# Optimization experiments

Measured on AMD Instinct MI355X. Metric: run time of the kernel, lower is better.

The kernel has to match this reference:

```python
import jax, jax.numpy as jnp
import numpy as np

B, T, HW = 16, 64, 7
D = 768          # input_dim == base_dim
N = 12           # num_heads
C = D // N       # head_dim = 64
EPS = 1e-5


def layernorm(x, g, b):
    m = jnp.mean(x, axis=-1, keepdims=True)
    v = jnp.mean((x - m) ** 2, axis=-1, keepdims=True)
    return (x - m) * jax.lax.rsqrt(v + EPS) * g + b


def setup_inputs() -> dict:
    key = jax.random.key(0)
    ks = jax.random.split(key, 12)
    s = lambda k, shape: (jax.random.normal(k, shape, jnp.float32) * 0.02)
    return {
        "x": jax.random.normal(ks[0], (B, T, HW, HW, D), jnp.float32),
        "W_qkv": s(ks[1], (D, 3 * D)),                  # qkv_bias=False
        "Wpq": s(ks[2], (C, C, HW, HW)), "bpq": jnp.zeros((C,), jnp.float32),
        "Wpk": s(ks[3], (C, C, HW, HW)), "bpk": jnp.zeros((C,), jnp.float32),
        "Wpv": s(ks[4], (C, C, HW, HW)), "bpv": jnp.zeros((C,), jnp.float32),
        "g_q": jnp.ones((C,), jnp.float32), "be_q": jnp.zeros((C,), jnp.float32),
        "g_k": jnp.ones((C,), jnp.float32), "be_k": jnp.zeros((C,), jnp.float32),
        "g_v": jnp.ones((C,), jnp.float32), "be_v": jnp.zeros((C,), jnp.float32),
        "rel_pos_t": s(ks[5], (2 * T - 1, C)),          # (127, 64): matches dt, no interp
        "W_proj": s(ks[6], (D, D)), "b_proj": jnp.zeros((D,), jnp.float32),
    }


def reference(x, W_qkv, Wpq, bpq, Wpk, bpk, Wpv, bpv,
              g_q, be_q, g_k, be_k, g_v, be_v, rel_pos_t, W_proj, b_proj):
    b, t = x.shape[0], x.shape[1]
    # qkv projection -> (B,T,H,W,3,N,C)
    qkv = (x @ W_qkv).reshape(b, t, HW, HW, 3, N, C)
    q3, k3, v3 = qkv[..., 0, :, :], qkv[..., 1, :, :], qkv[..., 2, :, :]  # (B,T,H,W,N,C)
    # Conv3d kernel (1,7,7) on full 7x7 spatial == contraction over (h,w,c_in)
    q = jnp.einsum('bthwnc,dchw->bntd', q3, Wpq) + bpq   # (B,N,T,C)
    k = jnp.einsum('bthwnc,dchw->bntd', k3, Wpk) + bpk
    v = jnp.einsum('bthwnc,dchw->bntd', v3, Wpv) + bpv
    q = layernorm(q, g_q, be_q)
    k = layernorm(k, g_k, be_k)
    v = layernorm(v, g_v, be_v)
    scale = C ** -0.5
    attn = jnp.einsum('bntc,bnsc->bnts', q * scale, k)   # (B,N,T,T)
    # relative temporal position bias: gather table rows by distance, matmul with q
    dist = jnp.arange(t)[:, None] - jnp.arange(t)[None, :] + (t - 1)  # (T,T) in [0,2T-2]
    Rt = rel_pos_t[dist]                                  # (T,T,C)
    rel = jnp.einsum('bntc,tsc->bnts', q, Rt)
    attn = jax.nn.softmax(attn + rel, axis=-1)
    out = jnp.einsum('bnts,bnsc->bntc', attn, v) + q      # residual add of q
    out = out.transpose(0, 2, 1, 3).reshape(b, t, N * C)  # (B,T,D)
    return out @ W_proj + b_proj
```

## Files before the change

kernel.cpp:

```cpp
#include <hip/hip_runtime.h>


typedef __attribute__((ext_vector_type(8))) short bf16x8;
typedef __attribute__((ext_vector_type(4))) float f32x4;

#define AS1U(p) ((const __attribute__((address_space(1))) unsigned int*)(p))
#define AS3U(p) ((__attribute__((address_space(3))) unsigned int*)(p))

__device__ __forceinline__ unsigned short cvt_bf16(float x) {
  union { float f; unsigned int u; } v; v.f = x;
  unsigned int r = v.u + 0x7fffu + ((v.u >> 16) & 1u);
  return (unsigned short)(r >> 16);
}
__device__ __forceinline__ float bf2f(unsigned short h) {
  union { unsigned int u; float f; } v; v.u = ((unsigned int)h) << 16;
  return v.f;
}

__global__ __launch_bounds__(256) void cvt_x_k(const float* __restrict__ src,
                                               unsigned short* __restrict__ dst, int n8) {
  int i = blockIdx.x * 256 + threadIdx.x;
  if (i >= n8) return;
  const float4* s = (const float4*)src + (size_t)i * 2;
  float4 a = s[0], b = s[1];
  ushort4 r0 = { cvt_bf16(a.x), cvt_bf16(a.y), cvt_bf16(a.z), cvt_bf16(a.w) };
  ushort4 r1 = { cvt_bf16(b.x), cvt_bf16(b.y), cvt_bf16(b.z), cvt_bf16(b.w) };
  ushort4* d = (ushort4*)dst + (size_t)i * 2;
  d[0] = r0; d[1] = r1;
}

__global__ __launch_bounds__(256) void transpose_cvt_k(const float* __restrict__ src,
                                                       unsigned short* __restrict__ dst) {
  __shared__ float tl[32][33];
  int k0 = blockIdx.x * 32, n0 = blockIdx.y * 32;
  int tx = threadIdx.x & 31, ty = threadIdx.x >> 5;
#pragma unroll
  for (int r = 0; r < 32; r += 8)
    tl[ty + r][tx] = src[(size_t)(k0 + ty + r) * 2304 + n0 + tx];
  __syncthreads();
#pragma unroll
  for (int r = 0; r < 32; r += 8)
    dst[(size_t)(n0 + ty + r) * 768 + k0 + tx] = cvt_bf16(tl[tx][ty + r]);
}

__global__ __launch_bounds__(256) void wp_cvt_k(const float* __restrict__ src,
                                                unsigned short* __restrict__ dst) {
  int o = blockIdx.x * 256 + threadIdx.x;
  if (o >= 204800) return;
  int c = o & 63, d = (o >> 6) & 63, hw = o >> 12;
  dst[o] = (hw < 49) ? cvt_bf16(src[d * 3136 + c * 49 + hw]) : (unsigned short)0;
}

__global__ __launch_bounds__(256) void relp_cvt_k(const float* __restrict__ src,
                                                  unsigned short* __restrict__ dst) {
  int i = blockIdx.x * 256 + threadIdx.x;
  if (i >= 8192) return;
  dst[i] = (i < 8128) ? cvt_bf16(src[i]) : (unsigned short)0;
}

__global__ __launch_bounds__(256) void gemm_qkv_k(
    const unsigned short* __restrict__ A, const unsigned short* __restrict__ Bt,
    unsigned short* __restrict__ Cb) {
  __shared__ unsigned short As[128 * 32];
  __shared__ unsigned short Bs[128 * 32];
  const int L = blockIdx.x;
  const int xcd = L & 7;
  const int slot = L >> 3;
  const int nb = slot % 18;
  const int mb = xcd * 49 + slot / 18;
  const int m0 = mb * 128, n0 = nb * 128;
  const int K = 768, Nn = 2304;

  const int tid = threadIdx.x;
  const int wave = tid >> 6, lane = tid & 63;
  const int quad = lane >> 4, l16 = lane & 15;
  const int wm = (wave >> 1) * 64, wn = (wave & 1) * 64;

  const int srow = lane >> 2;
  const int scol = (lane & 3) * 8;
  const unsigned short* Ag0 = A + (size_t)(m0 + wave * 16 + srow) * K + scol;
  const unsigned short* Ag1 = Ag0 + (size_t)64 * K;
  const unsigned short* Bg0 = Bt + (size_t)(n0 + wave * 16 + srow) * K + scol;
  const unsigned short* Bg1 = Bg0 + (size_t)64 * K;
  unsigned short* Asw0 = &As[(wave * 16) * 32];
  unsigned short* Asw1 = &As[(64 + wave * 16) * 32];
  unsigned short* Bsw0 = &Bs[(wave * 16) * 32];
  unsigned short* Bsw1 = &Bs[(64 + wave * 16) * 32];

  f32x4 acc[4][4];
#pragma unroll
  for (int i = 0; i < 4; ++i)
#pragma unroll
    for (int j = 0; j < 4; ++j) acc[i][j] = (f32x4){0.f, 0.f, 0.f, 0.f};

  for (int k0 = 0; k0 < K; k0 += 32) {
    __builtin_amdgcn_global_load_lds(AS1U(Ag0 + k0), AS3U(Asw0), 16, 0, 0);
    __builtin_amdgcn_global_load_lds(AS1U(Ag1 + k0), AS3U(Asw1), 16, 0, 0);
    __builtin_amdgcn_global_load_lds(AS1U(Bg0 + k0), AS3U(Bsw0), 16, 0, 0);
    __builtin_amdgcn_global_load_lds(AS1U(Bg1 + k0), AS3U(Bsw1), 16, 0, 0);
    __syncthreads();
    bf16x8 af[4], bfr[4];
#pragma unroll
    for (int f = 0; f < 4; ++f) {
      af[f]  = *(const bf16x8*)&As[(wm + f * 16 + l16) * 32 + quad * 8];
      bfr[f] = *(const bf16x8*)&Bs[(wn + f * 16 + l16) * 32 + quad * 8];
    }
#pragma unroll
    for (int i = 0; i < 4; ++i)
#pragma unroll
      for (int j = 0; j < 4; ++j)
        acc[i][j] = __builtin_amdgcn_mfma_f32_16x16x32_bf16(af[i], bfr[j], acc[i][j], 0, 0, 0);
    __syncthreads();
  }

#pragma unroll
  for (int i = 0; i < 4; ++i)
#pragma unroll
    for (int j = 0; j < 4; ++j)
#pragma unroll
      for (int r = 0; r < 4; ++r) {
        int row = m0 + wm + i * 16 + quad * 4 + r;
        int col = n0 + wn + j * 16 + l16;
        Cb[(size_t)row * Nn + col] = cvt_bf16(acc[i][j][r]);
      }
}

__global__ __launch_bounds__(256) void pool_ln_mfma_k(
    const unsigned short* __restrict__ qkvb, const unsigned short* __restrict__ WpTT,
    const float* __restrict__ bq, const float* __restrict__ bk, const float* __restrict__ bv,
    const float* __restrict__ gq, const float* __restrict__ gk, const float* __restrict__ gv,
    const float* __restrict__ beq, const float* __restrict__ bek, const float* __restrict__ bev,
    unsigned short* __restrict__ oq, unsigned short* __restrict__ ok_,
    unsigned short* __restrict__ ov) {
  __shared__ unsigned short As[64 * 128];
  __shared__ unsigned short Bs[64 * 128];
  __shared__ float Ln[64 * 65];
  __shared__ float mu_s[64], rs_s[64];

  const int n = blockIdx.x, p = blockIdx.y, b = blockIdx.z;
  const int tid = threadIdx.x;
  const int wave = tid >> 6, lane = tid & 63;
  const int quad = lane >> 4, l16 = lane & 15;
  const int wm = (wave >> 1) * 32, wn = (wave & 1) * 32;

  const int lr = lane >> 4, lg = lane & 15;
  const size_t abase = ((size_t)b * 3136) * 2304 + (size_t)p * 768 + (size_t)n * 64;
  const unsigned short* WpB = WpTT + (size_t)p * 204800;

  const unsigned short* pA[4];
  const unsigned short* pB[4];
#pragma unroll
  for (int q = 0; q < 4; ++q) {
    int r = wave * 16 + q * 4 + lr;
    int g = lg ^ (r & 15);
    pA[q] = qkvb + abase + (size_t)r * 112896 + (size_t)(g >> 3) * 2304 + (g & 7) * 8;
    pB[q] = WpB + (size_t)(g >> 3) * 4096 + r * 64 + (g & 7) * 8;
  }

  f32x4 acc[2][2];
#pragma unroll
  for (int i = 0; i < 2; ++i)
#pragma unroll
    for (int j = 0; j < 2; ++j) acc[i][j] = (f32x4){0.f, 0.f, 0.f, 0.f};

  for (int it = 0; it < 25; ++it) {
    const size_t offA = (size_t)it * 4608;
    const size_t offB = (size_t)it * 8192;
#pragma unroll
    for (int q = 0; q < 4; ++q) {
      __builtin_amdgcn_global_load_lds(AS1U(pA[q] + offA), AS3U(&As[(wave * 16 + q * 4) * 128]), 16, 0, 0);
      __builtin_amdgcn_global_load_lds(AS1U(pB[q] + offB), AS3U(&Bs[(wave * 16 + q * 4) * 128]), 16, 0, 0);
    }
    __syncthreads();
    bf16x8 af[2][4], bfr[2][4];
#pragma unroll
    for (int f = 0; f < 2; ++f) {
      int ra = wm + f * 16 + l16;
      int rb = wn + f * 16 + l16;
#pragma unroll
      for (int ki = 0; ki < 4; ++ki) {
        af[f][ki]  = *(const bf16x8*)&As[ra * 128 + (((ki * 4 + quad) ^ (ra & 15)) * 8)];
        bfr[f][ki] = *(const bf16x8*)&Bs[rb * 128 + (((ki * 4 + quad) ^ (rb & 15)) * 8)];
      }
    }
#pragma unroll
    for (int ki = 0; ki < 4; ++ki)
#pragma unroll
      for (int i = 0; i < 2; ++i)
#pragma unroll
        for (int j = 0; j < 2; ++j)
          acc[i][j] = __builtin_amdgcn_mfma_f32_16x16x32_bf16(af[i][ki], bfr[j][ki], acc[i][j], 0, 0, 0);
    __syncthreads();
  }

  const float* bias = (p == 0) ? bq : (p == 1) ? bk : bv;
  const float* g    = (p == 0) ? gq : (p == 1) ? gk : gv;
  const float* be   = (p == 0) ? beq : (p == 1) ? bek : bev;
  unsigned short* outp = (p == 0) ? oq : (p == 1) ? ok_ : ov;

#pragma unroll
  for (int i = 0; i < 2; ++i)
#pragma unroll
    for (int j = 0; j < 2; ++j)
#pragma unroll
      for (int r = 0; r < 4; ++r) {
        int t = wm + i * 16 + quad * 4 + r;
        int d = wn + j * 16 + l16;
        Ln[t * 65 + d] = acc[i][j][r] + bias[d];
      }
  __syncthreads();
  if (tid < 64) {
    float s = 0.f;
#pragma unroll 8
    for (int c = 0; c < 64; ++c) s += Ln[tid * 65 + c];
    float m = s * (1.f / 64.f);
    float v2 = 0.f;
#pragma unroll 8
    for (int c = 0; c < 64; ++c) { float dl = Ln[tid * 65 + c] - m; v2 += dl * dl; }
    mu_s[tid] = m;
    rs_s[tid] = rsqrtf(v2 * (1.f / 64.f) + 1e-5f);
  }
  __syncthreads();
  {
    int t = tid >> 2, d0 = (tid & 3) * 16;
    float m = mu_s[t], rv = rs_s[t];
    unsigned short ob[16];
#pragma unroll
    for (int j = 0; j < 16; ++j)
      ob[j] = cvt_bf16((Ln[t * 65 + d0 + j] - m) * rv * g[d0 + j] + be[d0 + j]);
    unsigned short* dst = outp + ((size_t)(b * 12 + n) * 64 + t) * 64 + d0;
    *(uint4*)dst = *(uint4*)ob;
    *(uint4*)(dst + 8) = *(uint4*)(ob + 8);
  }
}

__global__ __launch_bounds__(256) void attn_mfma_k(
    const unsigned short* __restrict__ qp, const unsigned short* __restrict__ kp,
    const unsigned short* __restrict__ vp, const unsigned short* __restrict__ relb,
    float* __restrict__ aout) {
  __shared__ unsigned short qs[64 * 64];
  __shared__ unsigned short ks[64 * 64];
  __shared__ unsigned short vt[64 * 64];
  __shared__ unsigned short rs[128 * 64];
  __shared__ float Gs[64 * 128];
  __shared__ unsigned short Ps[64 * 64];

  const int n = blockIdx.x, b = blockIdx.y;
  const int tid = threadIdx.x;
  const size_t base = ((size_t)b * 12 + n) * 4096;

  for (int i = tid; i < 512; i += 256) {
    ((uint4*)qs)[i] = ((const uint4*)(qp + base))[i];
    ((uint4*)ks)[i] = ((const uint4*)(kp + base))[i];
  }
  for (int i = tid; i < 1024; i += 256)
    ((uint4*)rs)[i] = ((const uint4*)relb)[i];
  {
    int s = tid >> 2, c0 = (tid & 3) * 16;
    unsigned short tmp[16];
    *(uint4*)tmp = *(const uint4*)(vp + base + s * 64 + c0);
    *(uint4*)(tmp + 8) = *(const uint4*)(vp + base + s * 64 + c0 + 8);
#pragma unroll
    for (int i = 0; i < 16; ++i) vt[(c0 + i) * 64 + s] = tmp[i];
  }
  __syncthreads();

  const int wave = tid >> 6, lane = tid & 63;
  const int quad = lane >> 4, l16 = lane & 15;
  const int tm = wave * 16;

  bf16x8 aq[2];
  aq[0] = *(const bf16x8*)&qs[(tm + l16) * 64 + quad * 8];
  aq[1] = *(const bf16x8*)&qs[(tm + l16) * 64 + quad * 8 + 32];

  f32x4 accqk[4], accg[8];
#pragma unroll
  for (int j = 0; j < 4; ++j) accqk[j] = (f32x4){0.f, 0.f, 0.f, 0.f};
#pragma unroll
  for (int j = 0; j < 8; ++j) accg[j] = (f32x4){0.f, 0.f, 0.f, 0.f};

#pragma unroll
  for (int ki = 0; ki < 2; ++ki) {
#pragma unroll
    for (int j = 0; j < 4; ++j) {
      bf16x8 bk = *(const bf16x8*)&ks[(j * 16 + l16) * 64 + quad * 8 + ki * 32];
      accqk[j] = __builtin_amdgcn_mfma_f32_16x16x32_bf16(aq[ki], bk, accqk[j], 0, 0, 0);
    }
#pragma unroll
    for (int j = 0; j < 8; ++j) {
      bf16x8 br = *(const bf16x8*)&rs[(j * 16 + l16) * 64 + quad * 8 + ki * 32];
      accg[j] = __builtin_amdgcn_mfma_f32_16x16x32_bf16(aq[ki], br, accg[j], 0, 0, 0);
    }
  }
#pragma unroll
  for (int j = 0; j < 8; ++j)
#pragma unroll
    for (int r = 0; r < 4; ++r)
      Gs[(tm + quad * 4 + r) * 128 + j * 16 + l16] = accg[j][r];
  __syncthreads();

#pragma unroll
  for (int r = 0; r < 4; ++r) {
    int t = tm + quad * 4 + r;
    float sv[4];
#pragma unroll
    for (int j = 0; j < 4; ++j) {
      int s = j * 16 + l16;
      sv[j] = 0.125f * accqk[j][r] + Gs[t * 128 + (t + 63 - s)];
    }
    float m = fmaxf(fmaxf(sv[0], sv[1]), fmaxf(sv[2], sv[3]));
    m = fmaxf(m, __shfl_xor(m, 1));
    m = fmaxf(m, __shfl_xor(m, 2));
    m = fmaxf(m, __shfl_xor(m, 4));
    m = fmaxf(m, __shfl_xor(m, 8));
    float e[4], sum = 0.f;
#pragma unroll
    for (int j = 0; j < 4; ++j) { e[j] = __expf(sv[j] - m); sum += e[j]; }
    sum += __shfl_xor(sum, 1);
    sum += __shfl_xor(sum, 2);
    sum += __shfl_xor(sum, 4);
    sum += __shfl_xor(sum, 8);
    float inv = 1.f / sum;
#pragma unroll
    for (int j = 0; j < 4; ++j)
      Ps[t * 64 + j * 16 + l16] = cvt_bf16(e[j] * inv);
  }
  __syncthreads();

  bf16x8 ap[2];
  ap[0] = *(const bf16x8*)&Ps[(tm + l16) * 64 + quad * 8];
  ap[1] = *(const bf16x8*)&Ps[(tm + l16) * 64 + quad * 8 + 32];
  f32x4 acco[4];
#pragma unroll
  for (int j = 0; j < 4; ++j) acco[j] = (f32x4){0.f, 0.f, 0.f, 0.f};
#pragma unroll
  for (int ki = 0; ki < 2; ++ki)
#pragma unroll
    for (int j = 0; j < 4; ++j) {
      bf16x8 bv = *(const bf16x8*)&vt[(j * 16 + l16) * 64 + quad * 8 + ki * 32];
      acco[j] = __builtin_amdgcn_mfma_f32_16x16x32_bf16(ap[ki], bv, acco[j], 0, 0, 0);
    }
#pragma unroll
  for (int j = 0; j < 4; ++j)
#pragma unroll
    for (int r = 0; r < 4; ++r) {
      int t = tm + quad * 4 + r;
      int c = j * 16 + l16;
      float o = acco[j][r] + bf2f(qs[t * 64 + c]);
      aout[((size_t)b * 64 + t) * 768 + n * 64 + c] = o;
    }
}

__global__ __launch_bounds__(256) void gemm_f32_k(
    const float* __restrict__ A, const float* __restrict__ Bm,
    const float* __restrict__ bias, float* __restrict__ Cm,
    int M, int Nn, int K) {
  __shared__ float As[16][68];
  __shared__ float Bs[16][64];
  const int tid = threadIdx.x;
  const int ty = tid >> 4, tx = tid & 15;
  const int m0 = blockIdx.y * 64, n0 = blockIdx.x * 64;

  const int la_m = tid >> 2;
  const int la_k = (tid & 3) << 2;
  const int lb_k = tid >> 4;
  const int lb_n = (tid & 15) << 2;

  const float* Ap = A + (size_t)(m0 + la_m) * K + la_k;
  const float* Bp = Bm + (size_t)lb_k * Nn + n0 + lb_n;

  float acc[4][4];
#pragma unroll
  for (int i = 0; i < 4; ++i)
#pragma unroll
    for (int j = 0; j < 4; ++j) acc[i][j] = 0.f;

  for (int k0 = 0; k0 < K; k0 += 16) {
    float4 av = *(const float4*)(Ap + k0);
    float4 bv = *(const float4*)(Bp + (size_t)k0 * Nn);
    As[la_k + 0][la_m] = av.x;
    As[la_k + 1][la_m] = av.y;
    As[la_k + 2][la_m] = av.z;
    As[la_k + 3][la_m] = av.w;
    *(float4*)&Bs[lb_k][lb_n] = bv;
    __syncthreads();
#pragma unroll
    for (int kk = 0; kk < 16; ++kk) {
      float af[4], bf[4];
      *(float4*)af = *(const float4*)&As[kk][ty << 2];
      *(float4*)bf = *(const float4*)&Bs[kk][tx << 2];
#pragma unroll
      for (int i = 0; i < 4; ++i)
#pragma unroll
        for (int j = 0; j < 4; ++j) acc[i][j] += af[i] * bf[j];
    }
    __syncthreads();
  }

  float bb[4] = {0.f, 0.f, 0.f, 0.f};
  if (bias) {
#pragma unroll
    for (int j = 0; j < 4; ++j) bb[j] = bias[n0 + (tx << 2) + j];
  }
#pragma unroll
  for (int i = 0; i < 4; ++i) {
    float4 o;
    o.x = acc[i][0] + bb[0];
    o.y = acc[i][1] + bb[1];
    o.z = acc[i][2] + bb[2];
    o.w = acc[i][3] + bb[3];
    *(float4*)(Cm + (size_t)(m0 + (ty << 2) + i) * Nn + n0 + (tx << 2)) = o;
  }
}

extern "C" void kernel_launch(void* const* d_in, const int* in_sizes, int n_in,
                              void* d_out, int out_size, void* d_ws, size_t ws_size,
                              hipStream_t stream) {
  const float* x     = (const float*)d_in[0];
  const float* Wqkv  = (const float*)d_in[1];
  const float* Wpq   = (const float*)d_in[2];
  const float* bpq   = (const float*)d_in[3];
  const float* Wpk   = (const float*)d_in[4];
  const float* bpk   = (const float*)d_in[5];
  const float* Wpv   = (const float*)d_in[6];
  const float* bpv   = (const float*)d_in[7];
  const float* gq    = (const float*)d_in[8];
  const float* beq   = (const float*)d_in[9];
  const float* gk    = (const float*)d_in[10];
  const float* bek   = (const float*)d_in[11];
  const float* gv    = (const float*)d_in[12];
  const float* bev   = (const float*)d_in[13];
  const float* relp  = (const float*)d_in[14];
  const float* Wproj = (const float*)d_in[15];
  const float* bproj = (const float*)d_in[16];
  float* out = (float*)d_out;

  unsigned short* u = (unsigned short*)d_ws;
  unsigned short* xbf   = u;
  unsigned short* qkvbf = u + 38535168ull;
  unsigned short* WqkvT = u + 154140672ull;
  unsigned short* WpTT  = u + 155910144ull;
  unsigned short* relb  = u + 156524544ull;
  unsigned short* qpb   = u + 156532736ull;
  unsigned short* kpb   = u + 157319168ull;
  unsigned short* vpb   = u + 158105600ull;
  float* aout = (float*)(u + 158892032ull);

  cvt_x_k<<<18816, 256, 0, stream>>>(x, xbf, 4816896);
  transpose_cvt_k<<<dim3(24, 72), 256, 0, stream>>>(Wqkv, WqkvT);
  wp_cvt_k<<<800, 256, 0, stream>>>(Wpq, WpTT);
  wp_cvt_k<<<800, 256, 0, stream>>>(Wpk, WpTT + 204800);
  wp_cvt_k<<<800, 256, 0, stream>>>(Wpv, WpTT + 409600);
  relp_cvt_k<<<32, 256, 0, stream>>>(relp, relb);

  gemm_qkv_k<<<7056, 256, 0, stream>>>(xbf, WqkvT, qkvbf);

  pool_ln_mfma_k<<<dim3(12, 3, 16), 256, 0, stream>>>(
      qkvbf, WpTT, bpq, bpk, bpv, gq, gk, gv, beq, bek, bev, qpb, kpb, vpb);

  attn_mfma_k<<<dim3(12, 16), 256, 0, stream>>>(qpb, kpb, vpb, relb, aout);

  gemm_f32_k<<<dim3(12, 16), 256, 0, stream>>>(aout, Wproj, bproj, out, 1024, 768, 768);
}
```

Measured before the change: 632.1 us.

## Rewrite QKV GEMM as 256x256 double-buffered 8-wave pipelined kernel

Replaces the 128x128, K=32, single-buffered QKV GEMM with a 512-thread 256x256 tile kernel. It uses K=64 stages, double-buffered LDS with an XOR swizzle, and interleaves global_load_lds prefetch with four MFMA quadrants separated by barriers and setprio. The aim is to hide global load latency, avoid LDS bank conflicts and raise arithmetic intensity per tile, using an XCD-aware block remap. In exchange it needs far more registers and LDS (128KB per block), which may limit occupancy, and it relies on hand-placed waitcnt and barrier ordering.

Measured after the change: 614.6 us. -2.8%, faster.

```diff
diff --git a/kernel.cpp b/kernel.cpp
--- a/kernel.cpp
+++ b/kernel.cpp
@@ -15,6 +15,12 @@
 __device__ __forceinline__ float bf2f(unsigned short h) {
   union { unsigned int u; float f; } v; v.u = ((unsigned int)h) << 16;
   return v.f;
+}
+
+__device__ __forceinline__ void wg_barrier() {
+  asm volatile("" ::: "memory");
+  __builtin_amdgcn_s_barrier();
+  asm volatile("" ::: "memory");
 }
 
 __global__ __launch_bounds__(256) void cvt_x_k(const float* __restrict__ src,
@@ -58,70 +64,139 @@
   dst[i] = (i < 8128) ? cvt_bf16(src[i]) : (unsigned short)0;
 }
 
-__global__ __launch_bounds__(256) void gemm_qkv_k(
+__global__ __launch_bounds__(512, 2) void gemm_qkv_8ph(
     const unsigned short* __restrict__ A, const unsigned short* __restrict__ Bt,
     unsigned short* __restrict__ Cb) {
-  __shared__ unsigned short As[128 * 32];
-  __shared__ unsigned short Bs[128 * 32];
-  const int L = blockIdx.x;
-  const int xcd = L & 7;
-  const int slot = L >> 3;
-  const int nb = slot % 18;
-  const int mb = xcd * 49 + slot / 18;
-  const int m0 = mb * 128, n0 = nb * 128;
-  const int K = 768, Nn = 2304;
+  __shared__ unsigned short As[2][16384];
+  __shared__ unsigned short Bs[2][16384];
+
+  const int orig = blockIdx.x;
+  const int xcd = orig & 7;
+  const int lid = orig >> 3;
+  const int wgid = (xcd < 4 ? xcd * 221 : 884 + (xcd - 4) * 220) + lid;
+  const int mb = wgid / 9, nb = wgid % 9;
+  const int m0 = mb * 256, n0 = nb * 256;
+  const int K = 768;
 
   const int tid = threadIdx.x;
   const int wave = tid >> 6, lane = tid & 63;
   const int quad = lane >> 4, l16 = lane & 15;
-  const int wm = (wave >> 1) * 64, wn = (wave & 1) * 64;
-
-  const int srow = lane >> 2;
-  const int scol = (lane & 3) * 8;
-  const unsigned short* Ag0 = A + (size_t)(m0 + wave * 16 + srow) * K + scol;
-  const unsigned short* Ag1 = Ag0 + (size_t)64 * K;
-  const unsigned short* Bg0 = Bt + (size_t)(n0 + wave * 16 + srow) * K + scol;
-  const unsigned short* Bg1 = Bg0 + (size_t)64 * K;
-  unsigned short* Asw0 = &As[(wave * 16) * 32];
-  unsigned short* Asw1 = &As[(64 + wave * 16) * 32];
-  unsigned short* Bsw0 = &Bs[(wave * 16) * 32];
-  unsigned short* Bsw1 = &Bs[(64 + wave * 16) * 32];
-
-  f32x4 acc[4][4];
-#pragma unroll
-  for (int i = 0; i < 4; ++i)
+  const int wr = wave >> 2, wc = wave & 3;
+  const int x7 = l16 & 7;
+
+  const int srow = tid >> 3;
+  const int cs = (tid & 7) ^ (srow & 7);
+  const unsigned short* Ag[4];
+  const unsigned short* Bg[4];
+#pragma unroll
+  for (int l = 0; l < 4; ++l) {
+    Ag[l] = A + (size_t)(m0 + l * 64 + srow) * K + cs * 8;
+    Bg[l] = Bt + (size_t)(n0 + l * 64 + srow) * K + cs * 8;
+  }
+  const int ldst = wave * 512;
+
+#define STAGE(buf, kt) do {                                                        \
+    const int ko_ = (kt) * 64;                                                     \
+    _Pragma("unroll")                                                              \
+    for (int l_ = 0; l_ < 4; ++l_) {                                               \
+      __builtin_amdgcn_global_load_lds(AS1U(Ag[l_] + ko_),                         \
+          AS3U(&As[buf][l_ * 4096 + ldst]), 16, 0, 0);                             \
+      __builtin_amdgcn_global_load_lds(AS1U(Bg[l_] + ko_),                         \
+          AS3U(&Bs[buf][l_ * 4096 + ldst]), 16, 0, 0);                             \
+    }                                                                              \
+  } while (0)
+
+#define LDA(buf, mi) do {                                                          \
+    _Pragma("unroll")                                                              \
+    for (int fi_ = 0; fi_ < 4; ++fi_) {                                            \
+      const int row_ = wr * 128 + (mi) * 64 + fi_ * 16 + l16;                      \
+      _Pragma("unroll")                                                            \
+      for (int ks_ = 0; ks_ < 2; ++ks_)                                            \
+        af[fi_][ks_] = *(const bf16x8*)&As[buf][row_ * 64 +                        \
+            (((ks_ * 4 + quad) ^ x7) * 8)];                                        \
+    }                                                                              \
+  } while (0)
+
+#define LDB(buf, nj) do {                                                          \
+    _Pragma("unroll")                                                              \
+    for (int fj_ = 0; fj_ < 2; ++fj_) {                                            \
+      const int row_ = wc * 64 + (nj) * 32 + fj_ * 16 + l16;                       \
+      _Pragma("unroll")                                                            \
+      for (int ks_ = 0; ks_ < 2; ++ks_)                                            \
+        bfv[nj][fj_][ks_] = *(const bf16x8*)&Bs[buf][row_ * 64 +                   \
+            (((ks_ * 4 + quad) ^ x7) * 8)];                                        \
+    }                                                                              \
+  } while (0)
+
+#define MFMAQ(mi, nj) do {                                                         \
+    _Pragma("unroll")                                                              \
+    for (int ks_ = 0; ks_ < 2; ++ks_)                                              \
+      _Pragma("unroll")                                                            \
+      for (int fi_ = 0; fi_ < 4; ++fi_)                                            \
+        _Pragma("unroll")                                                          \
+        for (int fj_ = 0; fj_ < 2; ++fj_)                                          \
+          acc[(mi) * 4 + fi_][(nj) * 2 + fj_] =                                    \
+              __builtin_amdgcn_mfma_f32_16x16x32_bf16(af[fi_][ks_],                \
+                  bfv[nj][fj_][ks_], acc[(mi) * 4 + fi_][(nj) * 2 + fj_], 0, 0, 0);\
+  } while (0)
+
+#define ITER(cur, DO_STAGE, kt2, VMI) do {                                         \
+    asm volatile("s_waitcnt vmcnt(" #VMI ")" ::: "memory");                        \
+    wg_barrier();                                                                  \
+                                                                           \
+    LDA(cur, 0); LDB(cur, 0);                                                      \
+    wg_barrier();                                                                  \
+    __builtin_amdgcn_s_setprio(1); MFMAQ(0, 0); __builtin_amdgcn_s_setprio(0);     \
+    wg_barrier();                                                                  \
+                                                                           \
+    LDB(cur, 1);                                                                   \
+    wg_barrier();                                                                  \
+    __builtin_amdgcn_s_setprio(1); MFMAQ(0, 1); __builtin_amdgcn_s_setprio(0);     \
+    wg_barrier();                                                                  \
+                                                                           \
+    LDA(cur, 1);                                                                   \
+    wg_barrier();                                                                  \
+    __builtin_amdgcn_s_setprio(1); MFMAQ(1, 0); __builtin_amdgcn_s_setprio(0);     \
+    wg_barrier();                                                                  \
+             \
+    if (DO_STAGE) STAGE(cur, kt2);                                                 \
+    __builtin_amdgcn_s_setprio(1); MFMAQ(1, 1); __builtin_amdgcn_s_setprio(0);     \
+    wg_barrier();                                                                  \
+  } while (0)
+
+  f32x4 acc[8][4];
+#pragma unroll
+  for (int i = 0; i < 8; ++i)
 #pragma unroll
     for (int j = 0; j < 4; ++j) acc[i][j] = (f32x4){0.f, 0.f, 0.f, 0.f};
-
-  for (int k0 = 0; k0 < K; k0 += 32) {
-    __builtin_amdgcn_global_load_lds(AS1U(Ag0 + k0), AS3U(Asw0), 16, 0, 0);
-    __builtin_amdgcn_global_load_lds(AS1U(Ag1 + k0), AS3U(Asw1), 16, 0, 0);
-    __builtin_amdgcn_global_load_lds(AS1U(Bg0 + k0), AS3U(Bsw0), 16, 0, 0);
-    __builtin_amdgcn_global_load_lds(AS1U(Bg1 + k0), AS3U(Bsw1), 16, 0, 0);
-    __syncthreads();
-    bf16x8 af[4], bfr[4];
-#pragma unroll
-    for (int f = 0; f < 4; ++f) {
-      af[f]  = *(const bf16x8*)&As[(wm + f * 16 + l16) * 32 + quad * 8];
-      bfr[f] = *(const bf16x8*)&Bs[(wn + f * 16 + l16) * 32 + quad * 8];
-    }
-#pragma unroll
-    for (int i = 0; i < 4; ++i)
-#pragma unroll
-      for (int j = 0; j < 4; ++j)
-        acc[i][j] = __builtin_amdgcn_mfma_f32_16x16x32_bf16(af[i], bfr[j], acc[i][j], 0, 0, 0);
-    __syncthreads();
-  }
-
-#pragma unroll
-  for (int i = 0; i < 4; ++i)
+  bf16x8 af[4][2];
+  bf16x8 bfv[2][2][2];
+
+  STAGE(0, 0);
+  STAGE(1, 1);
+
+  for (int kt = 0; kt < 10; kt += 2) {
+    ITER(0, true, kt + 2, 8);
+    ITER(1, true, kt + 3, 8);
+  }
+  ITER(0, false, 0, 8);
+  ITER(1, false, 0, 0);
+
+#undef ITER
+#undef MFMAQ
+#undef LDB
+#undef LDA
+#undef STAGE
+
+#pragma unroll
+  for (int i = 0; i < 8; ++i)
 #pragma unroll
     for (int j = 0; j < 4; ++j)
 #pragma unroll
       for (int r = 0; r < 4; ++r) {
-        int row = m0 + wm + i * 16 + quad * 4 + r;
-        int col = n0 + wn + j * 16 + l16;
-        Cb[(size_t)row * Nn + col] = cvt_bf16(acc[i][j][r]);
+        int row = m0 + wr * 128 + i * 16 + quad * 4 + r;
+        int col = n0 + wc * 64 + j * 16 + l16;
+        Cb[(size_t)row * 2304 + col] = cvt_bf16(acc[i][j][r]);
       }
 }
 
@@ -453,7 +528,7 @@
   wp_cvt_k<<<800, 256, 0, stream>>>(Wpv, WpTT + 409600);
   relp_cvt_k<<<32, 256, 0, stream>>>(relp, relb);
 
-  gemm_qkv_k<<<7056, 256, 0, stream>>>(xbf, WqkvT, qkvbf);
+  gemm_qkv_8ph<<<1764, 512, 0, stream>>>(xbf, WqkvT, qkvbf);
 
   pool_ln_mfma_k<<<dim3(12, 3, 16), 256, 0, stream>>>(
       qkvbf, WpTT, bpq, bpk, bpv, gq, gk, gv, beq, bek, bev, qpb, kpb, vpb);
```
